# Performance work log

Hardware: AMD Instinct MI355X
Metric: run time of the kernel (lower is better)

The kernel has to match this reference:

```python
import jax, jax.numpy as jnp
from jax import lax
import numpy as np

B, S, D, H = 16, 4096, 256, 256


def setup_inputs() -> dict:
    key = jax.random.key(0)
    k1, k2, k3, k4 = jax.random.split(key, 4)
    scale_x = 1.0 / np.sqrt(D)
    scale_h = 1.0 / np.sqrt(H)
    return {
        "inputs": jax.random.normal(k1, (B, S, D), dtype=jnp.float32),
        "state0": jnp.zeros((B, H), dtype=jnp.float32),
        "Wx": jax.random.normal(k2, (D, H), dtype=jnp.float32) * scale_x,
        "Wh": jax.random.normal(k3, (H, H), dtype=jnp.float32) * scale_h,
        "b": jnp.zeros((H,), dtype=jnp.float32),
    }


def reference(inputs, state0, Wx, Wh, b):
    # inputs: [B, S, D] -> time-major [S, B, D] (mirrors inputs.transpose_(0,1))
    x_tm = jnp.transpose(inputs, (1, 0, 2))
    # Precompute the input projection for all timesteps in one GEMM
    x_proj = jnp.einsum("sbd,dh->sbh", x_tm, Wx) + b  # [S, B, H]

    def step(h, xp_t):
        h_new = jnp.tanh(xp_t + h @ Wh)  # cell update; get_output = identity
        return h_new, h_new  # dropout p=0.0 -> identity

    _, outs = lax.scan(step, state0, x_proj)  # outs: [S, B, H]
    return jnp.transpose(outs, (1, 0, 2))  # back to [B, S, H]
```

## Files before the change

kernel.cpp:

```cpp
#include <hip/hip_runtime.h>

#define B_ 16
#define S_ 4096
#define D_ 256
#define H_ 256

typedef _Float16 h2 __attribute__((ext_vector_type(2)));
typedef _Float16 h4 __attribute__((ext_vector_type(4)));
typedef _Float16 h8 __attribute__((ext_vector_type(8)));
typedef _Float16 h8v __attribute__((ext_vector_type(8)));
typedef float f4 __attribute__((ext_vector_type(4)));

static __device__ __forceinline__ float fdot2f(h2 a, h2 b, float c) {
    return __builtin_amdgcn_fdot2(a, b, c, false);
}

template <int CTRL>
static __device__ __forceinline__ float dpp_qp(float v) {
    int r = __builtin_amdgcn_update_dpp(0, __float_as_int(v), CTRL, 0xF, 0xF, true);
    return __int_as_float(r);
}
#define DPP_XOR1 0xB1
#define DPP_XOR2 0x4E

static __device__ __forceinline__ void lds_barrier() {
    asm volatile("s_waitcnt lgkmcnt(0)" ::: "memory");
    __builtin_amdgcn_s_barrier();
}

static __device__ __forceinline__ int swz(int i) {
    const int s = i >> 6, r = (i >> 3) & 7, e = i & 7;
    return 64 * s + 8 * ((r + 2 * s) & 7) + e;
}

__global__ __launch_bounds__(256, 1) void xproj_kernel(
    const float* __restrict__ x, const float* __restrict__ Wx,
    const float* __restrict__ bias, float* __restrict__ out)
{
    __shared__ __align__(16) _Float16 xs[16 * 272];
    const int tid = threadIdx.x;
    const int l   = tid & 63;
    const int wav = tid >> 6;
    const int lc  = l & 15;
    const int kg  = l >> 4;
    const long long row0 = (long long)blockIdx.x * 256;

    h8v bf[4][8];
    #pragma unroll
    for (int nt = 0; nt < 4; ++nt) {
        const int j = 64 * wav + 16 * nt + lc;
        #pragma unroll
        for (int ks = 0; ks < 8; ++ks) {
            #pragma unroll
            for (int e = 0; e < 8; ++e)
                bf[nt][ks][e] = (_Float16)Wx[(32 * ks + 8 * kg + e) * H_ + j];
        }
    }
    float bvv[4];
    #pragma unroll
    for (int nt = 0; nt < 4; ++nt)
        bvv[nt] = bias[64 * wav + 16 * nt + lc];

    f4 pre[4];
    #pragma unroll
    for (int k4 = 0; k4 < 4; ++k4)
        pre[k4] = *(const f4*)&x[(row0 + wav + 4 * k4) * D_ + 4 * l];

    for (int it = 0; it < 16; ++it) {
        const long long r0 = row0 + it * 16;

        __syncthreads();
        #pragma unroll
        for (int k4 = 0; k4 < 4; ++k4) {
            h4 hv;
            hv[0] = (_Float16)pre[k4].x;
            hv[1] = (_Float16)pre[k4].y;
            hv[2] = (_Float16)pre[k4].z;
            hv[3] = (_Float16)pre[k4].w;
            *(h4*)&xs[(wav + 4 * k4) * 272 + 4 * l] = hv;
        }
        __syncthreads();

        if (it + 1 < 16) {
            const long long rn = row0 + (it + 1) * 16;
            #pragma unroll
            for (int k4 = 0; k4 < 4; ++k4)
                pre[k4] = *(const f4*)&x[(rn + wav + 4 * k4) * D_ + 4 * l];
        }

        f4 acc[4];
        #pragma unroll
        for (int nt = 0; nt < 4; ++nt)
            acc[nt] = (f4){0.f, 0.f, 0.f, 0.f};

        #pragma unroll
        for (int ks = 0; ks < 8; ++ks) {
            h8v af = *(const h8v*)&xs[lc * 272 + 32 * ks + 8 * kg];
            acc[0] = __builtin_amdgcn_mfma_f32_16x16x32_f16(af, bf[0][ks], acc[0], 0, 0, 0);
            acc[1] = __builtin_amdgcn_mfma_f32_16x16x32_f16(af, bf[1][ks], acc[1], 0, 0, 0);
            acc[2] = __builtin_amdgcn_mfma_f32_16x16x32_f16(af, bf[2][ks], acc[2], 0, 0, 0);
            acc[3] = __builtin_amdgcn_mfma_f32_16x16x32_f16(af, bf[3][ks], acc[3], 0, 0, 0);
        }

        #pragma unroll
        for (int nt = 0; nt < 4; ++nt) {
            const int j = 64 * wav + 16 * nt + lc;
            #pragma unroll
            for (int r = 0; r < 4; ++r)
                out[(r0 + 4 * kg + r) * H_ + j] = acc[nt][r] + bvv[nt];
        }
    }
}

__global__ __launch_bounds__(256, 1) void scan_kernel(
    const float* __restrict__ Wh, const float* __restrict__ state0,
    float* __restrict__ out)
{
    __shared__ __align__(16) _Float16 hbuf[2][H_];
    const int tid = threadIdx.x;
    const int s = tid & 3;
    const int q = tid >> 2;
    const int b = blockIdx.x;
    const bool o1 = (s & 1) != 0;
    const bool o2 = (s & 2) != 0;

    h2 w[4][32];
    #pragma unroll
    for (int jj = 0; jj < 4; ++jj) {
        const int j = 4 * q + jj;
        #pragma unroll
        for (int ii = 0; ii < 32; ++ii) {
            const int i = 64 * s + 2 * ii;
            h2 p;
            p[0] = (_Float16)Wh[(long long)i * H_ + j];
            p[1] = (_Float16)Wh[(long long)(i + 1) * H_ + j];
            w[jj][ii] = p;
        }
    }

    hbuf[0][swz(tid)] = (_Float16)state0[b * H_ + tid];

    float* __restrict__ outb = out + (long long)b * S_ * H_;

    float xr[4];
    #pragma unroll
    for (int k = 0; k < 4; ++k)
        xr[k] = outb[(long long)k * H_ + tid];
    __syncthreads();

    #pragma unroll 4
    for (int st = 0; st < S_; ++st) {
        const int p = st & 1;
        const _Float16* hb = hbuf[p];

        h8 hv[8];
        #pragma unroll
        for (int r = 0; r < 8; ++r)
            hv[r] = *(const h8*)&hb[64 * s + 8 * ((r + 2 * s) & 7)];

        float acc0 = 0.f, acc1 = 0.f, acc2 = 0.f, acc3 = 0.f;
        #pragma unroll
        for (int r = 0; r < 8; ++r) {
            union { h8 v; h2 pr[4]; } u;
            u.v = hv[r];
            #pragma unroll
            for (int m = 0; m < 4; ++m) {
                const int ii = 4 * r + m;
                acc0 = fdot2f(u.pr[m], w[0][ii], acc0);
                acc1 = fdot2f(u.pr[m], w[1][ii], acc1);
                acc2 = fdot2f(u.pr[m], w[2][ii], acc2);
                acc3 = fdot2f(u.pr[m], w[3][ii], acc3);
            }
        }

        float vA = o1 ? acc1 : acc0;
        float vB = o1 ? acc3 : acc2;
        float sA = o1 ? acc0 : acc1;
        float sB = o1 ? acc2 : acc3;
        vA += dpp_qp<DPP_XOR1>(sA);
        vB += dpp_qp<DPP_XOR1>(sB);
        float v   = o2 ? vB : vA;
        float snd = o2 ? vA : vB;
        v += dpp_qp<DPP_XOR2>(snd);

        const float pre = v + xr[st & 3];
        const float e = __builtin_amdgcn_exp2f(pre * 2.8853900817779268f);
        const float hn = fmaf(-2.f, __builtin_amdgcn_rcpf(e + 1.f), 1.f);

        outb[(long long)st * H_ + tid] = hn;
        hbuf[p ^ 1][swz(tid)] = (_Float16)hn;

        const int nt = st + 4;
        xr[st & 3] = (nt < S_) ? outb[(long long)nt * H_ + tid] : 0.f;
        lds_barrier();
    }
}

extern "C" void kernel_launch(void* const* d_in, const int* in_sizes, int n_in,
                              void* d_out, int out_size, void* d_ws, size_t ws_size,
                              hipStream_t stream) {
    const float* x  = (const float*)d_in[0];
    const float* s0 = (const float*)d_in[1];
    const float* Wx = (const float*)d_in[2];
    const float* Wh = (const float*)d_in[3];
    const float* bv = (const float*)d_in[4];
    float* out = (float*)d_out;

    xproj_kernel<<<dim3((B_ * S_) / 256), dim3(256), 0, stream>>>(x, Wx, bv, out);
    scan_kernel<<<dim3(B_), dim3(256), 0, stream>>>(Wh, s0, out);
}
```

Measured before the change: 1.704 ms.

## Process two batch rows per scan block to amortize per-step latency

```diff
diff --git a/kernel.cpp b/kernel.cpp
--- a/kernel.cpp
+++ b/kernel.cpp
@@ -116,13 +116,15 @@
     const float* __restrict__ Wh, const float* __restrict__ state0,
     float* __restrict__ out)
 {
-    __shared__ __align__(16) _Float16 hbuf[2][H_];
+    __shared__ __align__(16) _Float16 hbufA[2][H_];
+    __shared__ __align__(16) _Float16 hbufB[2][H_];
     const int tid = threadIdx.x;
     const int s = tid & 3;
     const int q = tid >> 2;
-    const int b = blockIdx.x;
     const bool o1 = (s & 1) != 0;
     const bool o2 = (s & 2) != 0;
+    const int bA = blockIdx.x * 2;
+    const int bB = bA + 1;
 
     h2 w[4][32];
     #pragma unroll
@@ -138,60 +140,85 @@
         }
     }
 
-    hbuf[0][swz(tid)] = (_Float16)state0[b * H_ + tid];
-
-    float* __restrict__ outb = out + (long long)b * S_ * H_;
-
-    float xr[4];
-    #pragma unroll
-    for (int k = 0; k < 4; ++k)
-        xr[k] = outb[(long long)k * H_ + tid];
+    hbufA[0][swz(tid)] = (_Float16)state0[bA * H_ + tid];
+    hbufB[0][swz(tid)] = (_Float16)state0[bB * H_ + tid];
+
+    float* __restrict__ outA = out + (long long)bA * S_ * H_;
+    float* __restrict__ outB = out + (long long)bB * S_ * H_;
+
+    float xrA[4], xrB[4];
+    #pragma unroll
+    for (int k = 0; k < 4; ++k) {
+        xrA[k] = outA[(long long)k * H_ + tid];
+        xrB[k] = outB[(long long)k * H_ + tid];
+    }
     __syncthreads();
 
-    #pragma unroll 4
+    #pragma unroll 2
     for (int st = 0; st < S_; ++st) {
         const int p = st & 1;
-        const _Float16* hb = hbuf[p];
-
-        h8 hv[8];
+        const _Float16* hbA = hbufA[p];
+        const _Float16* hbB = hbufB[p];
+
+        h8 hvA[8], hvB[8];
         #pragma unroll
         for (int r = 0; r < 8; ++r)
-            hv[r] = *(const h8*)&hb[64 * s + 8 * ((r + 2 * s) & 7)];
-
-        float acc0 = 0.f, acc1 = 0.f, acc2 = 0.f, acc3 = 0.f;
+            hvA[r] = *(const h8*)&hbA[64 * s + 8 * ((r + 2 * s) & 7)];
+        #pragma unroll
+        for (int r = 0; r < 8; ++r)
+            hvB[r] = *(const h8*)&hbB[64 * s + 8 * ((r + 2 * s) & 7)];
+
+        float aA0 = 0.f, aA1 = 0.f, aA2 = 0.f, aA3 = 0.f;
+        float aB0 = 0.f, aB1 = 0.f, aB2 = 0.f, aB3 = 0.f;
         #pragma unroll
         for (int r = 0; r < 8; ++r) {
-            union { h8 v; h2 pr[4]; } u;
-            u.v = hv[r];
+            union { h8 v; h2 pr[4]; } uA, uB;
+            uA.v = hvA[r];
+            uB.v = hvB[r];
             #pragma unroll
             for (int m = 0; m < 4; ++m) {
                 const int ii = 4 * r + m;
-                acc0 = fdot2f(u.pr[m], w[0][ii], acc0);
-                acc1 = fdot2f(u.pr[m], w[1][ii], acc1);
-                acc2 = fdot2f(u.pr[m], w[2][ii], acc2);
-                acc3 = fdot2f(u.pr[m], w[3][ii], acc3);
+                aA0 = fdot2f(uA.pr[m], w[0][ii], aA0);
+                aA1 = fdot2f(uA.pr[m], w[1][ii], aA1);
+                aA2 = fdot2f(uA.pr[m], w[2][ii], aA2);
+                aA3 = fdot2f(uA.pr[m], w[3][ii], aA3);
+                aB0 = fdot2f(uB.pr[m], w[0][ii], aB0);
+                aB1 = fdot2f(uB.pr[m], w[1][ii], aB1);
+                aB2 = fdot2f(uB.pr[m], w[2][ii], aB2);
+                aB3 = fdot2f(uB.pr[m], w[3][ii], aB3);
             }
         }
 
-        float vA = o1 ? acc1 : acc0;
-        float vB = o1 ? acc3 : acc2;
-        float sA = o1 ? acc0 : acc1;
-        float sB = o1 ? acc2 : acc3;
-        vA += dpp_qp<DPP_XOR1>(sA);
-        vB += dpp_qp<DPP_XOR1>(sB);
-        float v   = o2 ? vB : vA;
-        float snd = o2 ? vA : vB;
-        v += dpp_qp<DPP_XOR2>(snd);
-
-        const float pre = v + xr[st & 3];
-        const float e = __builtin_amdgcn_exp2f(pre * 2.8853900817779268f);
-        const float hn = fmaf(-2.f, __builtin_amdgcn_rcpf(e + 1.f), 1.f);
-
-        outb[(long long)st * H_ + tid] = hn;
-        hbuf[p ^ 1][swz(tid)] = (_Float16)hn;
+        float vA1 = o1 ? aA1 : aA0, sA1 = o1 ? aA0 : aA1;
+        float vA2 = o1 ? aA3 : aA2, sA2 = o1 ? aA2 : aA3;
+        vA1 += dpp_qp<DPP_XOR1>(sA1);
+        vA2 += dpp_qp<DPP_XOR1>(sA2);
+        float vA  = o2 ? vA2 : vA1, dA = o2 ? vA1 : vA2;
+        vA += dpp_qp<DPP_XOR2>(dA);
+        float vB1 = o1 ? aB1 : aB0, sB1 = o1 ? aB0 : aB1;
+        float vB2 = o1 ? aB3 : aB2, sB2 = o1 ? aB2 : aB3;
+        vB1 += dpp_qp<DPP_XOR1>(sB1);
+        vB2 += dpp_qp<DPP_XOR1>(sB2);
+        float vB  = o2 ? vB2 : vB1, dB = o2 ? vB1 : vB2;
+        vB += dpp_qp<DPP_XOR2>(dB);
+
+        const float preA = vA + xrA[st & 3];
+        const float preB = vB + xrB[st & 3];
+        const float eA = __builtin_amdgcn_exp2f(preA * 2.8853900817779268f);
+        const float eB = __builtin_amdgcn_exp2f(preB * 2.8853900817779268f);
+        const float hnA = fmaf(-2.f, __builtin_amdgcn_rcpf(eA + 1.f), 1.f);
+        const float hnB = fmaf(-2.f, __builtin_amdgcn_rcpf(eB + 1.f), 1.f);
+
+        outA[(long long)st * H_ + tid] = hnA;
+        outB[(long long)st * H_ + tid] = hnB;
+        hbufA[p ^ 1][swz(tid)] = (_Float16)hnA;
+        hbufB[p ^ 1][swz(tid)] = (_Float16)hnB;
 
         const int nt = st + 4;
-        xr[st & 3] = (nt < S_) ? outb[(long long)nt * H_ + tid] : 0.f;
+        if (nt < S_) {
+            xrA[st & 3] = outA[(long long)nt * H_ + tid];
+            xrB[st & 3] = outB[(long long)nt * H_ + tid];
+        }
         lds_barrier();
     }
 }
@@ -207,5 +234,5 @@
     float* out = (float*)d_out;
 
     xproj_kernel<<<dim3((B_ * S_) / 256), dim3(256), 0, stream>>>(x, Wx, bv, out);
-    scan_kernel<<<dim3(B_), dim3(256), 0, stream>>>(Wh, s0, out);
-}
+    scan_kernel<<<dim3(B_ / 2), dim3(256), 0, stream>>>(Wh, s0, out);
+}
```

After: 4.237 ms. +148.7%, slower.

## Split recurrent matvec between MFMA waves and dot2 VALU waves in one block

Applied to the files above, without the earlier changes.

```diff
diff --git a/kernel.cpp b/kernel.cpp
--- a/kernel.cpp
+++ b/kernel.cpp
@@ -22,6 +22,7 @@
 }
 #define DPP_XOR1 0xB1
 #define DPP_XOR2 0x4E
+#define DPP_ROR8 0x128
 
 static __device__ __forceinline__ void lds_barrier() {
     asm volatile("s_waitcnt lgkmcnt(0)" ::: "memory");
@@ -31,6 +32,10 @@
 static __device__ __forceinline__ int swz(int i) {
     const int s = i >> 6, r = (i >> 3) & 7, e = i & 7;
     return 64 * s + 8 * ((r + 2 * s) & 7) + e;
+}
+static __device__ __forceinline__ int swz_chunk(int c) {
+    const int s = c >> 3, r = c & 7;
+    return 64 * s + 8 * ((r + 2 * s) & 7);
 }
 
 __global__ __launch_bounds__(256, 1) void xproj_kernel(
@@ -112,87 +117,149 @@
     }
 }
 
-__global__ __launch_bounds__(256, 1) void scan_kernel(
+__global__ __launch_bounds__(512, 1) void scan_kernel(
     const float* __restrict__ Wh, const float* __restrict__ state0,
     float* __restrict__ out)
 {
     __shared__ __align__(16) _Float16 hbuf[2][H_];
-    const int tid = threadIdx.x;
-    const int s = tid & 3;
-    const int q = tid >> 2;
+    const int tid0 = threadIdx.x;
     const int b = blockIdx.x;
-    const bool o1 = (s & 1) != 0;
-    const bool o2 = (s & 2) != 0;
-
-    h2 w[4][32];
-    #pragma unroll
-    for (int jj = 0; jj < 4; ++jj) {
-        const int j = 4 * q + jj;
-        #pragma unroll
-        for (int ii = 0; ii < 32; ++ii) {
-            const int i = 64 * s + 2 * ii;
-            h2 p;
-            p[0] = (_Float16)Wh[(long long)i * H_ + j];
-            p[1] = (_Float16)Wh[(long long)(i + 1) * H_ + j];
-            w[jj][ii] = p;
-        }
-    }
-
-    hbuf[0][swz(tid)] = (_Float16)state0[b * H_ + tid];
-
     float* __restrict__ outb = out + (long long)b * S_ * H_;
 
-    float xr[4];
-    #pragma unroll
-    for (int k = 0; k < 4; ++k)
-        xr[k] = outb[(long long)k * H_ + tid];
-    __syncthreads();
-
-    #pragma unroll 4
-    for (int st = 0; st < S_; ++st) {
-        const int p = st & 1;
-        const _Float16* hb = hbuf[p];
-
-        h8 hv[8];
-        #pragma unroll
-        for (int r = 0; r < 8; ++r)
-            hv[r] = *(const h8*)&hb[64 * s + 8 * ((r + 2 * s) & 7)];
-
-        float acc0 = 0.f, acc1 = 0.f, acc2 = 0.f, acc3 = 0.f;
-        #pragma unroll
-        for (int r = 0; r < 8; ++r) {
-            union { h8 v; h2 pr[4]; } u;
-            u.v = hv[r];
-            #pragma unroll
-            for (int m = 0; m < 4; ++m) {
-                const int ii = 4 * r + m;
-                acc0 = fdot2f(u.pr[m], w[0][ii], acc0);
-                acc1 = fdot2f(u.pr[m], w[1][ii], acc1);
-                acc2 = fdot2f(u.pr[m], w[2][ii], acc2);
-                acc3 = fdot2f(u.pr[m], w[3][ii], acc3);
-            }
-        }
-
-        float vA = o1 ? acc1 : acc0;
-        float vB = o1 ? acc3 : acc2;
-        float sA = o1 ? acc0 : acc1;
-        float sB = o1 ? acc2 : acc3;
-        vA += dpp_qp<DPP_XOR1>(sA);
-        vB += dpp_qp<DPP_XOR1>(sB);
-        float v   = o2 ? vB : vA;
-        float snd = o2 ? vA : vB;
-        v += dpp_qp<DPP_XOR2>(snd);
-
-        const float pre = v + xr[st & 3];
-        const float e = __builtin_amdgcn_exp2f(pre * 2.8853900817779268f);
-        const float hn = fmaf(-2.f, __builtin_amdgcn_rcpf(e + 1.f), 1.f);
-
-        outb[(long long)st * H_ + tid] = hn;
-        hbuf[p ^ 1][swz(tid)] = (_Float16)hn;
-
-        const int nt = st + 4;
-        xr[st & 3] = (nt < S_) ? outb[(long long)nt * H_ + tid] : 0.f;
-        lds_barrier();
+    if (tid0 < 256) {
+        const int l   = tid0 & 63;
+        const int wav = tid0 >> 6;
+        const int lc  = l & 15;
+        const int kg  = l >> 4;
+        const int j_m = 32 * wav + 16 * kg + lc;
+        const bool own = (kg < 2);
+
+        h8v bf[2][8];
+        #pragma unroll
+        for (int nt = 0; nt < 2; ++nt) {
+            const int j = 32 * wav + 16 * nt + lc;
+            #pragma unroll
+            for (int ks = 0; ks < 8; ++ks) {
+                #pragma unroll
+                for (int e = 0; e < 8; ++e)
+                    bf[nt][ks][e] = (_Float16)Wh[(32 * ks + 8 * kg + e) * H_ + j];
+            }
+        }
+        int abase[8];
+        #pragma unroll
+        for (int ks = 0; ks < 8; ++ks)
+            abase[ks] = swz_chunk(4 * ks + kg);
+
+        hbuf[0][swz(tid0)] = (_Float16)state0[b * H_ + tid0];
+
+        float xr[4];
+        #pragma unroll
+        for (int k = 0; k < 4; ++k)
+            xr[k] = outb[(long long)k * H_ + j_m];
+        __syncthreads();
+
+        #pragma unroll 4
+        for (int st = 0; st < S_; ++st) {
+            const int p = st & 1;
+            const _Float16* hb = hbuf[p];
+
+            f4 acc0 = {0.f, 0.f, 0.f, 0.f};
+            f4 acc1 = {0.f, 0.f, 0.f, 0.f};
+            #pragma unroll
+            for (int ks = 0; ks < 8; ++ks) {
+                h8v af = *(const h8v*)&hb[abase[ks]];
+                acc0 = __builtin_amdgcn_mfma_f32_16x16x32_f16(af, bf[0][ks], acc0, 0, 0, 0);
+                acc1 = __builtin_amdgcn_mfma_f32_16x16x32_f16(af, bf[1][ks], acc1, 0, 0, 0);
+            }
+
+            const float v = (kg == 1) ? acc1[0] : acc0[0];
+            const float pre = v + xr[st & 3];
+            const float e = __builtin_amdgcn_exp2f(pre * 2.8853900817779268f);
+            const float hn = fmaf(-2.f, __builtin_amdgcn_rcpf(e + 1.f), 1.f);
+
+            if (own) {
+                outb[(long long)st * H_ + j_m] = hn;
+                hbuf[p ^ 1][swz(j_m)] = (_Float16)hn;
+            }
+            const int nt4 = st + 4;
+            if (nt4 < S_) xr[st & 3] = outb[(long long)nt4 * H_ + j_m];
+            lds_barrier();
+        }
+    } else {
+        const int t  = tid0 - 256;
+        const int sl = (t & 3) | ((t >> 1) & 4);
+        const int g  = ((t >> 2) & 1) | ((t >> 4) << 1);
+        const bool s1 = (sl & 1) != 0, s2 = (sl & 2) != 0;
+        const bool own = (t & 8) == 0;
+        const int j_v = 128 + 4 * g + (t & 3);
+
+        h2 w[4][16];
+        #pragma unroll
+        for (int jj = 0; jj < 4; ++jj) {
+            const int j = 128 + 4 * g + jj;
+            #pragma unroll
+            for (int pp = 0; pp < 16; ++pp) {
+                const int i = 32 * sl + 2 * pp;
+                h2 q;
+                q[0] = (_Float16)Wh[(long long)i * H_ + j];
+                q[1] = (_Float16)Wh[(long long)(i + 1) * H_ + j];
+                w[jj][pp] = q;
+            }
+        }
+        int raddr[4];
+        #pragma unroll
+        for (int k = 0; k < 4; ++k)
+            raddr[k] = swz_chunk(4 * sl + k);
+
+        float xr[4];
+        #pragma unroll
+        for (int k = 0; k < 4; ++k)
+            xr[k] = outb[(long long)k * H_ + j_v];
+        __syncthreads();
+
+        #pragma unroll 4
+        for (int st = 0; st < S_; ++st) {
+            const int p = st & 1;
+            const _Float16* hb = hbuf[p];
+
+            union { h8 v; h2 q[4]; } u[4];
+            #pragma unroll
+            for (int k = 0; k < 4; ++k)
+                u[k].v = *(const h8*)&hb[raddr[k]];
+
+            float a0 = 0.f, a1 = 0.f, a2 = 0.f, a3 = 0.f;
+            #pragma unroll
+            for (int k = 0; k < 4; ++k) {
+                #pragma unroll
+                for (int m = 0; m < 4; ++m) {
+                    const int ii = 4 * k + m;
+                    a0 = fdot2f(u[k].q[m], w[0][ii], a0);
+                    a1 = fdot2f(u[k].q[m], w[1][ii], a1);
+                    a2 = fdot2f(u[k].q[m], w[2][ii], a2);
+                    a3 = fdot2f(u[k].q[m], w[3][ii], a3);
+                }
+            }
+
+            float k0 = s1 ? a1 : a0, d0 = s1 ? a0 : a1;
+            float k1 = s1 ? a3 : a2, d1 = s1 ? a2 : a3;
+            k0 += dpp_qp<DPP_XOR1>(d0);
+            k1 += dpp_qp<DPP_XOR1>(d1);
+            float n = s2 ? k1 : k0, e0 = s2 ? k0 : k1;
+            n += dpp_qp<DPP_XOR2>(e0);
+            n += dpp_qp<DPP_ROR8>(n);
+
+            const float pre = n + xr[st & 3];
+            const float e = __builtin_amdgcn_exp2f(pre * 2.8853900817779268f);
+            const float hn = fmaf(-2.f, __builtin_amdgcn_rcpf(e + 1.f), 1.f);
+
+            if (own) {
+                outb[(long long)st * H_ + j_v] = hn;
+                hbuf[p ^ 1][swz(j_v)] = (_Float16)hn;
+            }
+            const int nt4 = st + 4;
+            if (nt4 < S_) xr[st & 3] = outb[(long long)nt4 * H_ + j_v];
+            lds_barrier();
+        }
     }
 }
 
@@ -207,5 +274,5 @@
     float* out = (float*)d_out;
 
     xproj_kernel<<<dim3((B_ * S_) / 256), dim3(256), 0, stream>>>(x, Wx, bv, out);
-    scan_kernel<<<dim3(B_), dim3(256), 0, stream>>>(Wh, s0, out);
-}
+    scan_kernel<<<dim3(B_), dim3(512), 0, stream>>>(Wh, s0, out);
+}
```

Result: slower. 1.859 ms (+9.1%).
